# Kernel tuning notes

Measured on AMD Instinct MI355X. Metric: run time of the kernel, lower is better.

The kernel has to match this reference:

```python
import jax, jax.numpy as jnp
import numpy as np

B, S, I, H, C = 256, 128, 512, 1024, 10
VOCAB = S  # nn.Embedding(seq_length, input_dim)


def _lstm_dir(embeds_tbi, W, b):
    """Run an LSTM over time. embeds_tbi: [S,B,I]; W: [4H, I+H] stacked (g,i,f,o); b: [4H]."""
    h0 = jnp.zeros((B, H), jnp.float32)
    c0 = jnp.zeros((B, H), jnp.float32)

    def step(carry, x_t):
        c, h = carry
        xh = jnp.concatenate([x_t, h], axis=1)          # [B, I+H]
        z = xh @ W.T + b                                 # [B, 4H]
        g, i, f, o = jnp.split(z, 4, axis=1)
        g = jnp.tanh(g)
        i = jax.nn.sigmoid(i)
        f = jax.nn.sigmoid(f)
        o = jax.nn.sigmoid(o)
        new_c = g * i + c * f
        new_h = jnp.tanh(new_c) * o
        return (new_c, new_h), None

    (c_T, h_T), _ = jax.lax.scan(step, (c0, h0), embeds_tbi)
    return h_T


def setup_inputs() -> dict:
    key = jax.random.key(0)
    ks = jax.random.split(key, 8)
    x = jax.random.randint(ks[0], (B, S), 0, VOCAB)
    embed = jax.random.normal(ks[1], (VOCAB, I), jnp.float32) * 0.5
    scale = 1.0 / np.sqrt(I + H)
    fwd_W = jax.random.normal(ks[2], (4 * H, I + H), jnp.float32) * scale  # stacked g,i,f,o
    fwd_b = jax.random.normal(ks[3], (4 * H,), jnp.float32) * 0.02
    bwd_W = jax.random.normal(ks[4], (4 * H, I + H), jnp.float32) * scale
    bwd_b = jax.random.normal(ks[5], (4 * H,), jnp.float32) * 0.02
    p_w = jax.random.normal(ks[6], (C, 2 * H), jnp.float32) * (1.0 / np.sqrt(2 * H))
    p_b = jax.random.normal(ks[7], (C,), jnp.float32) * 0.02
    return {"x": x, "embed": embed, "fwd_W": fwd_W, "fwd_b": fwd_b,
            "bwd_W": bwd_W, "bwd_b": bwd_b, "p_w": p_w, "p_b": p_b}


def reference(x, embed, fwd_W, fwd_b, bwd_W, bwd_b, p_w, p_b):
    embeds = embed[x]                       # [B,S,I]
    emb_t = jnp.transpose(embeds, (1, 0, 2))  # [S,B,I]
    h_fwd = _lstm_dir(emb_t, fwd_W, fwd_b)
    h_bwd = _lstm_dir(emb_t[::-1], bwd_W, bwd_b)
    h_comb = jnp.concatenate([h_fwd, h_bwd], axis=1)  # [B,2H]
    return jax.nn.log_softmax(h_comb @ p_w.T + p_b, axis=1)
```

## Files before the change

### kernel.cpp

```cpp
#include <hip/hip_runtime.h>
#include <hip/hip_bf16.h>
#include <math.h>

#define B 256
#define S 128
#define I_DIM 512
#define H 1024
#define C 10
#define WROW 1536

#define LDS_H 131072

typedef float f32x4 __attribute__((ext_vector_type(4), may_alias));
typedef __bf16 bf16x8 __attribute__((ext_vector_type(8), may_alias));
typedef unsigned int u32x4 __attribute__((ext_vector_type(4), may_alias));
typedef unsigned long long u64;
typedef unsigned long long __attribute__((may_alias)) u64a;

__device__ __forceinline__ unsigned short f2bf(float f) {
    union { float f; unsigned u; } a; a.f = f;
    return (unsigned short)((a.u + 0x7fffu + ((a.u >> 16) & 1u)) >> 16);
}
__device__ __forceinline__ float bf2f(unsigned short b) {
    union { unsigned u; float f; } a; a.u = ((unsigned)b) << 16;
    return a.f;
}
__device__ __forceinline__ float sigf(float v) { return 1.0f / (1.0f + __expf(-v)); }
__device__ __forceinline__ float tanh_fast(float v) { return 1.0f - 2.0f / (1.0f + __expf(2.0f * v)); }

__global__ void wf_build(const float* __restrict__ fwd_W,
                         const float* __restrict__ bwd_W,
                         __hip_bfloat16* __restrict__ wF) {
    int gid = blockIdx.x * 256 + threadIdx.x;
    int lane = gid & 63, kk = (gid >> 6) & 31, nsub = (gid >> 11) & 255, d = gid >> 19;
    int n_gl = nsub * 16 + (lane & 15);
    int j = n_gl >> 2, g = n_gl & 3;
    int k = kk * 32 + (lane >> 4) * 8;
    const float* W = d ? bwd_W : fwd_W;
    const float* src = W + (size_t)(g * 1024 + j) * WROW + I_DIM + k;
    ushort4 lo = make_ushort4(f2bf(src[0]), f2bf(src[1]), f2bf(src[2]), f2bf(src[3]));
    ushort4 hi = make_ushort4(f2bf(src[4]), f2bf(src[5]), f2bf(src[6]), f2bf(src[7]));
    ushort4* dst = (ushort4*)(wF + (size_t)gid * 8);
    dst[0] = lo; dst[1] = hi;
}

__global__ void wxf_build(const float* __restrict__ fwd_W,
                          const float* __restrict__ bwd_W,
                          __hip_bfloat16* __restrict__ wxF) {
    int gid = blockIdx.x * 256 + threadIdx.x;
    int lane = gid & 63, kk = (gid >> 6) & 15, nsub = (gid >> 10) & 255, d = gid >> 18;
    int n_gl = nsub * 16 + (lane & 15);
    int j = n_gl >> 2, g = n_gl & 3;
    int k = kk * 32 + (lane >> 4) * 8;
    const float* W = d ? bwd_W : fwd_W;
    const float* src = W + (size_t)(g * 1024 + j) * WROW + k;
    ushort4 lo = make_ushort4(f2bf(src[0]), f2bf(src[1]), f2bf(src[2]), f2bf(src[3]));
    ushort4 hi = make_ushort4(f2bf(src[4]), f2bf(src[5]), f2bf(src[6]), f2bf(src[7]));
    ushort4* dst = (ushort4*)(wxF + (size_t)gid * 8);
    dst[0] = lo; dst[1] = hi;
}

__global__ void ehl_build(const float* __restrict__ embed,
                          unsigned short* __restrict__ ehl) {
    int idx = blockIdx.x * 256 + threadIdx.x;
    float e = embed[idx];
    unsigned short hb = f2bf(e);
    unsigned short lb = f2bf(e - bf2f(hb));
    ehl[idx] = hb;
    ehl[65536 + idx] = lb;
}

__global__ __launch_bounds__(256) void projp_mfma(
        const __hip_bfloat16* __restrict__ wxF,
        const unsigned short* __restrict__ ehl,
        const float* __restrict__ fwd_b,
        const float* __restrict__ bwd_b,
        float* __restrict__ projP) {
    extern __shared__ char sm[];
    const int bid = blockIdx.x;
    const int d = bid >> 7, jt = (bid >> 2) & 31, vb = bid & 3;
    const int tid = threadIdx.x, w = tid >> 6, lane = tid & 63;
    const int l15 = lane & 15, l4 = lane >> 4;
    const int v0 = vb * 32;

    for (int i = 0; i < 16; i++) {
        int chunk = i * 256 + tid;
        int row = chunk >> 6, c16 = chunk & 63;
        int p = row >> 5, vs = v0 + (row & 31);
        u32x4 vd = *(const u32x4*)(ehl + ((size_t)p * 128 + vs) * 512 + c16 * 8);
        *(u32x4*)(sm + row * 1024 + ((c16 * 16) ^ ((row & 7) << 4))) = vd;
    }
    __syncthreads();

    const __hip_bfloat16* ap0 = wxF + ((size_t)((d * 256 + jt * 8 + w * 2 + 0) * 16)) * 512;
    const __hip_bfloat16* ap1 = wxF + ((size_t)((d * 256 + jt * 8 + w * 2 + 1) * 16)) * 512;
    int hrow[2], hswz[2], lrow[2], lswz[2];
#pragma unroll
    for (int vt = 0; vt < 2; vt++) {
        int hr = vt * 16 + l15, lr = hr + 32;
        hrow[vt] = hr * 1024; hswz[vt] = (hr & 7) << 4;
        lrow[vt] = lr * 1024; lswz[vt] = (lr & 7) << 4;
    }
    f32x4 acc[2][2] = {};
#pragma unroll
    for (int kk = 0; kk < 16; kk++) {
        bf16x8 A0 = *(const bf16x8*)(ap0 + kk * 512 + lane * 8);
        bf16x8 A1 = *(const bf16x8*)(ap1 + kk * 512 + lane * 8);
        int ko = kk * 64 + l4 * 16;
        bf16x8 Bh0 = *(const bf16x8*)(sm + hrow[0] + (ko ^ hswz[0]));
        bf16x8 Bh1 = *(const bf16x8*)(sm + hrow[1] + (ko ^ hswz[1]));
        bf16x8 Bl0 = *(const bf16x8*)(sm + lrow[0] + (ko ^ lswz[0]));
        bf16x8 Bl1 = *(const bf16x8*)(sm + lrow[1] + (ko ^ lswz[1]));
        acc[0][0] = __builtin_amdgcn_mfma_f32_16x16x32_bf16(A0, Bh0, acc[0][0], 0, 0, 0);
        acc[0][0] = __builtin_amdgcn_mfma_f32_16x16x32_bf16(A0, Bl0, acc[0][0], 0, 0, 0);
        acc[0][1] = __builtin_amdgcn_mfma_f32_16x16x32_bf16(A0, Bh1, acc[0][1], 0, 0, 0);
        acc[0][1] = __builtin_amdgcn_mfma_f32_16x16x32_bf16(A0, Bl1, acc[0][1], 0, 0, 0);
        acc[1][0] = __builtin_amdgcn_mfma_f32_16x16x32_bf16(A1, Bh0, acc[1][0], 0, 0, 0);
        acc[1][0] = __builtin_amdgcn_mfma_f32_16x16x32_bf16(A1, Bl0, acc[1][0], 0, 0, 0);
        acc[1][1] = __builtin_amdgcn_mfma_f32_16x16x32_bf16(A1, Bh1, acc[1][1], 0, 0, 0);
        acc[1][1] = __builtin_amdgcn_mfma_f32_16x16x32_bf16(A1, Bl1, acc[1][1], 0, 0, 0);
    }
    const float* bp = d ? bwd_b : fwd_b;
#pragma unroll
    for (int nt = 0; nt < 2; nt++) {
        int j = jt * 32 + w * 8 + nt * 4 + l4;
        f32x4 bv = { bp[j], bp[1024 + j], bp[2048 + j], bp[3072 + j] };
#pragma unroll
        for (int vt = 0; vt < 2; vt++) {
            int v = v0 + vt * 16 + l15;
            *(f32x4*)(projP + ((size_t)(d * 1024 + j) * 128 + v) * 4) = acc[nt][vt] + bv;
        }
    }
}

__global__ __launch_bounds__(512, 1) void step_kernel(
        const int* __restrict__ x,
        const __hip_bfloat16* __restrict__ wF,
        const float* __restrict__ projP,
        __hip_bfloat16* __restrict__ hbuf,
        float* __restrict__ cws,
        int t) {
    extern __shared__ char smem[];
    const int bid = blockIdx.x;
    const int d = bid >> 7, bt = (bid >> 5) & 3, jt = bid & 31;
    const int tid = threadIdx.x, wid = tid >> 6, lane = tid & 63;
    const int l15 = lane & 15, l4 = lane >> 4;
    const int b0 = bt * 64;
    const size_t dBH = (size_t)d * B * H;

    if (t > 0) {
        const __hip_bfloat16* hr = hbuf + (size_t)(t & 1) * 2 * B * H + dBH + (size_t)b0 * H;
#pragma unroll
        for (int i = 0; i < 16; i++) {
            int flat = i * 512 + tid;
            int row = flat >> 7, c16 = flat & 127;
            u32x4 v = *(const u32x4*)(hr + (size_t)row * H + c16 * 8);
            *(u32x4*)(smem + row * 2048 + ((c16 * 16) ^ ((row & 7) << 4))) = v;
        }
        __syncthreads();
    }

    f32x4 acc[4] = {};
    if (t > 0) {
        const __hip_bfloat16* wp = wF + (size_t)(d * 256 + jt * 8 + wid) * 16384;
        int brow[4], bswz[4];
#pragma unroll
        for (int bs = 0; bs < 4; bs++) {
            int row = bs * 16 + l15;
            brow[bs] = row * 2048;
            bswz[bs] = (row & 7) << 4;
        }
        bf16x8 Acur = *(const bf16x8*)(wp + lane * 8);
        bf16x8 Bcur[4];
#pragma unroll
        for (int bs = 0; bs < 4; bs++)
            Bcur[bs] = *(const bf16x8*)(smem + brow[bs] + ((l4 * 16) ^ bswz[bs]));
#pragma unroll
        for (int kk = 0; kk < 32; kk++) {
            bf16x8 A = Acur;
            bf16x8 B0 = Bcur[0], B1 = Bcur[1], B2 = Bcur[2], B3 = Bcur[3];
            if (kk < 31) {
                Acur = *(const bf16x8*)(wp + (kk + 1) * 512 + lane * 8);
                int koff = (kk + 1) * 64 + l4 * 16;
#pragma unroll
                for (int bs = 0; bs < 4; bs++)
                    Bcur[bs] = *(const bf16x8*)(smem + brow[bs] + (koff ^ bswz[bs]));
            }
            acc[0] = __builtin_amdgcn_mfma_f32_16x16x32_bf16(A, B0, acc[0], 0, 0, 0);
            acc[1] = __builtin_amdgcn_mfma_f32_16x16x32_bf16(A, B1, acc[1], 0, 0, 0);
            acc[2] = __builtin_amdgcn_mfma_f32_16x16x32_bf16(A, B2, acc[2], 0, 0, 0);
            acc[3] = __builtin_amdgcn_mfma_f32_16x16x32_bf16(A, B3, acc[3], 0, 0, 0);
        }
    }

    const int tt = d ? (S - 1 - t) : t;
    const int j = jt * 32 + wid * 4 + l4;
    const f32x4* pp = (const f32x4*)projP + ((size_t)d * 1024 + j) * 128;
    f32x4 pj[4];
#pragma unroll
    for (int bs = 0; bs < 4; bs++) {
        int v = x[(b0 + bs * 16 + l15) * S + tt];
        pj[bs] = pp[v];
    }

    float* cp = cws + ((size_t)bid * 512 + tid) * 4;
    f32x4 cv = {0.f, 0.f, 0.f, 0.f};
    if (t > 0) cv = *(const f32x4*)cp;

    float hnv[4];
#pragma unroll
    for (int bs = 0; bs < 4; bs++) {
        float zg = acc[bs][0] + pj[bs][0];
        float zi = acc[bs][1] + pj[bs][1];
        float zf = acc[bs][2] + pj[bs][2];
        float zo = acc[bs][3] + pj[bs][3];
        float gg = tanh_fast(zg);
        float ii = sigf(zi);
        float ff = sigf(zf);
        float oo = sigf(zo);
        float cn = gg * ii + cv[bs] * ff;
        cv[bs] = cn;
        hnv[bs] = tanh_fast(cn) * oo;
    }
    *(f32x4*)cp = cv;

    unsigned plo = (unsigned)f2bf(hnv[0]) | ((unsigned)f2bf(hnv[1]) << 16);
    unsigned phi = (unsigned)f2bf(hnv[2]) | ((unsigned)f2bf(hnv[3]) << 16);
    unsigned short o4[4];
#pragma unroll
    for (int p = 0; p < 4; p++) {
        int src = p * 16 + l15;
        unsigned vlo = __shfl(plo, src);
        unsigned vhi = __shfl(phi, src);
        unsigned sel = (l4 < 2) ? vlo : vhi;
        o4[p] = (l4 & 1) ? (unsigned short)(sel >> 16) : (unsigned short)(sel & 0xffffu);
    }
    u64 hv = (u64)o4[0] | ((u64)o4[1] << 16) | ((u64)o4[2] << 32) | ((u64)o4[3] << 48);
    __hip_bfloat16* hw = hbuf + (size_t)((t + 1) & 1) * 2 * B * H + dBH
                         + (size_t)(b0 + lane) * H + jt * 32 + wid * 4;
    *(u64a*)hw = hv;
}

__global__ void head_kernel(const __hip_bfloat16* __restrict__ hbuf,
                            const float* __restrict__ p_w,
                            const float* __restrict__ p_b,
                            float* __restrict__ out) {
    int b = blockIdx.x;
    int lane = threadIdx.x;
    float part[C];
#pragma unroll
    for (int cc = 0; cc < C; cc++) part[cc] = 0.0f;
    for (int jj = lane; jj < 2 * H; jj += 64) {
        float hv = (jj < H)
            ? __bfloat162float(hbuf[(size_t)b * H + jj])
            : __bfloat162float(hbuf[(size_t)B * H + (size_t)b * H + jj - H]);
#pragma unroll
        for (int cc = 0; cc < C; cc++) part[cc] += hv * p_w[cc * 2 * H + jj];
    }
#pragma unroll
    for (int cc = 0; cc < C; cc++) {
        float v = part[cc];
        for (int off = 32; off; off >>= 1) v += __shfl_down(v, off);
        part[cc] = v;
    }
    if (lane == 0) {
        float lg[C];
        float m = -1e30f;
        for (int cc = 0; cc < C; cc++) {
            lg[cc] = part[cc] + p_b[cc];
            m = fmaxf(m, lg[cc]);
        }
        float s = 0.0f;
        for (int cc = 0; cc < C; cc++) s += expf(lg[cc] - m);
        float lse = logf(s) + m;
        for (int cc = 0; cc < C; cc++) out[b * C + cc] = lg[cc] - lse;
    }
}

extern "C" void kernel_launch(void* const* d_in, const int* in_sizes, int n_in,
                              void* d_out, int out_size, void* d_ws, size_t ws_size,
                              hipStream_t stream) {
    const int*   x     = (const int*)d_in[0];
    const float* embed = (const float*)d_in[1];
    const float* fwd_W = (const float*)d_in[2];
    const float* fwd_b = (const float*)d_in[3];
    const float* bwd_W = (const float*)d_in[4];
    const float* bwd_b = (const float*)d_in[5];
    const float* p_w   = (const float*)d_in[6];
    const float* p_b   = (const float*)d_in[7];
    float* outp = (float*)d_out;

    char* ws = (char*)d_ws;
    __hip_bfloat16* wF  = (__hip_bfloat16*)ws;  ws += (size_t)2 * 256 * 16384 * 2;
    __hip_bfloat16* wxF = (__hip_bfloat16*)ws;
    float* cws = (float*)ws;                    ws += (size_t)2 * 256 * 8192 * 2;
    unsigned short* ehl = (unsigned short*)ws;  ws += (size_t)2 * 128 * 512 * 2;
    float* projP = (float*)ws;                  ws += (size_t)2 * 1024 * 128 * 4 * 4;
    __hip_bfloat16* hbuf = (__hip_bfloat16*)ws; ws += (size_t)2 * 2 * B * H * 2;

    hipLaunchKernelGGL(wf_build, dim3(4096), dim3(256), 0, stream, fwd_W, bwd_W, wF);
    hipLaunchKernelGGL(wxf_build, dim3(2048), dim3(256), 0, stream, fwd_W, bwd_W, wxF);
    hipLaunchKernelGGL(ehl_build, dim3(256), dim3(256), 0, stream, embed, ehl);

    hipFuncSetAttribute((const void*)projp_mfma,
                        hipFuncAttributeMaxDynamicSharedMemorySize, 65536);
    hipLaunchKernelGGL(projp_mfma, dim3(256), dim3(256), 65536, stream,
                       wxF, ehl, fwd_b, bwd_b, projP);

    hipFuncSetAttribute((const void*)step_kernel,
                        hipFuncAttributeMaxDynamicSharedMemorySize, LDS_H);
    for (int t = 0; t < S; t++)
        hipLaunchKernelGGL(step_kernel, dim3(256), dim3(512), LDS_H, stream,
                           x, wF, projP, hbuf, cws, t);

    hipLaunchKernelGGL(head_kernel, dim3(B), dim3(64), 0, stream,
                       hbuf, p_w, p_b, outp);
}
```

Measured before the change: 1.431 ms.

## Load hidden state directly to LDS and merge prep kernels into one launch

The step kernel now stages the previous hidden-state tile into LDS with global_load_lds, which loads straight from global memory into LDS and skips the trip through registers. The XOR swizzle moves from the LDS write address to the global read address, because the direct-to-LDS path writes contiguous lane slots. The three weight/embedding preparation kernels are merged into one launch to save launch overhead. The step-kernel change runs 128 times and is the main target, but it relies on the builtin's LDS addressing semantics matching the assumed layout.

```diff
diff --git a/kernel.cpp b/kernel.cpp
--- a/kernel.cpp
+++ b/kernel.cpp
@@ -28,46 +28,44 @@
 __device__ __forceinline__ float sigf(float v) { return 1.0f / (1.0f + __expf(-v)); }
 __device__ __forceinline__ float tanh_fast(float v) { return 1.0f - 2.0f / (1.0f + __expf(2.0f * v)); }
 
-__global__ void wf_build(const float* __restrict__ fwd_W,
-                         const float* __restrict__ bwd_W,
-                         __hip_bfloat16* __restrict__ wF) {
+__global__ void prep_build(const float* __restrict__ fwd_W,
+                           const float* __restrict__ bwd_W,
+                           const float* __restrict__ embed,
+                           __hip_bfloat16* __restrict__ wF,
+                           __hip_bfloat16* __restrict__ wxF,
+                           unsigned short* __restrict__ ehl) {
     int gid = blockIdx.x * 256 + threadIdx.x;
-    int lane = gid & 63, kk = (gid >> 6) & 31, nsub = (gid >> 11) & 255, d = gid >> 19;
-    int n_gl = nsub * 16 + (lane & 15);
-    int j = n_gl >> 2, g = n_gl & 3;
-    int k = kk * 32 + (lane >> 4) * 8;
-    const float* W = d ? bwd_W : fwd_W;
-    const float* src = W + (size_t)(g * 1024 + j) * WROW + I_DIM + k;
-    ushort4 lo = make_ushort4(f2bf(src[0]), f2bf(src[1]), f2bf(src[2]), f2bf(src[3]));
-    ushort4 hi = make_ushort4(f2bf(src[4]), f2bf(src[5]), f2bf(src[6]), f2bf(src[7]));
-    ushort4* dst = (ushort4*)(wF + (size_t)gid * 8);
-    dst[0] = lo; dst[1] = hi;
-}
-
-__global__ void wxf_build(const float* __restrict__ fwd_W,
-                          const float* __restrict__ bwd_W,
-                          __hip_bfloat16* __restrict__ wxF) {
-    int gid = blockIdx.x * 256 + threadIdx.x;
-    int lane = gid & 63, kk = (gid >> 6) & 15, nsub = (gid >> 10) & 255, d = gid >> 18;
-    int n_gl = nsub * 16 + (lane & 15);
-    int j = n_gl >> 2, g = n_gl & 3;
-    int k = kk * 32 + (lane >> 4) * 8;
-    const float* W = d ? bwd_W : fwd_W;
-    const float* src = W + (size_t)(g * 1024 + j) * WROW + k;
-    ushort4 lo = make_ushort4(f2bf(src[0]), f2bf(src[1]), f2bf(src[2]), f2bf(src[3]));
-    ushort4 hi = make_ushort4(f2bf(src[4]), f2bf(src[5]), f2bf(src[6]), f2bf(src[7]));
-    ushort4* dst = (ushort4*)(wxF + (size_t)gid * 8);
-    dst[0] = lo; dst[1] = hi;
-}
-
-__global__ void ehl_build(const float* __restrict__ embed,
-                          unsigned short* __restrict__ ehl) {
-    int idx = blockIdx.x * 256 + threadIdx.x;
-    float e = embed[idx];
-    unsigned short hb = f2bf(e);
-    unsigned short lb = f2bf(e - bf2f(hb));
-    ehl[idx] = hb;
-    ehl[65536 + idx] = lb;
+    if (gid < 1048576) {
+        int lane = gid & 63, kk = (gid >> 6) & 31, nsub = (gid >> 11) & 255, d = gid >> 19;
+        int n_gl = nsub * 16 + (lane & 15);
+        int j = n_gl >> 2, g = n_gl & 3;
+        int k = kk * 32 + (lane >> 4) * 8;
+        const float* W = d ? bwd_W : fwd_W;
+        const float* src = W + (size_t)(g * 1024 + j) * WROW + I_DIM + k;
+        ushort4 lo = make_ushort4(f2bf(src[0]), f2bf(src[1]), f2bf(src[2]), f2bf(src[3]));
+        ushort4 hi = make_ushort4(f2bf(src[4]), f2bf(src[5]), f2bf(src[6]), f2bf(src[7]));
+        ushort4* dst = (ushort4*)(wF + (size_t)gid * 8);
+        dst[0] = lo; dst[1] = hi;
+    } else if (gid < 1048576 + 524288) {
+        int g2 = gid - 1048576;
+        int lane = g2 & 63, kk = (g2 >> 6) & 15, nsub = (g2 >> 10) & 255, d = g2 >> 18;
+        int n_gl = nsub * 16 + (lane & 15);
+        int j = n_gl >> 2, g = n_gl & 3;
+        int k = kk * 32 + (lane >> 4) * 8;
+        const float* W = d ? bwd_W : fwd_W;
+        const float* src = W + (size_t)(g * 1024 + j) * WROW + k;
+        ushort4 lo = make_ushort4(f2bf(src[0]), f2bf(src[1]), f2bf(src[2]), f2bf(src[3]));
+        ushort4 hi = make_ushort4(f2bf(src[4]), f2bf(src[5]), f2bf(src[6]), f2bf(src[7]));
+        ushort4* dst = (ushort4*)(wxF + (size_t)g2 * 8);
+        dst[0] = lo; dst[1] = hi;
+    } else {
+        int idx = gid - (1048576 + 524288);
+        float e = embed[idx];
+        unsigned short hb = f2bf(e);
+        unsigned short lb = f2bf(e - bf2f(hb));
+        ehl[idx] = hb;
+        ehl[65536 + idx] = lb;
+    }
 }
 
 __global__ __launch_bounds__(256) void projp_mfma(
@@ -149,14 +147,28 @@
     const size_t dBH = (size_t)d * B * H;
 
     if (t > 0) {
-        const __hip_bfloat16* hr = hbuf + (size_t)(t & 1) * 2 * B * H + dBH + (size_t)b0 * H;
+        const char* hrb = (const char*)(hbuf + (size_t)(t & 1) * 2 * B * H + dBH + (size_t)b0 * H);
+#if __has_builtin(__builtin_amdgcn_global_load_lds)
+#pragma unroll
+        for (int i = 0; i < 16; i++) {
+            int r = i * 8 + wid;
+            int row = r >> 1, half = r & 1;
+            int m = half * 64 + lane;
+            const void* src = hrb + row * 2048 + ((m ^ (row & 7)) << 4);
+            __builtin_amdgcn_global_load_lds(
+                (const __attribute__((address_space(1))) void*)src,
+                (__attribute__((address_space(3))) void*)(smem + row * 2048 + half * 1024),
+                16, 0, 0);
+        }
+#else
 #pragma unroll
         for (int i = 0; i < 16; i++) {
             int flat = i * 512 + tid;
             int row = flat >> 7, c16 = flat & 127;
-            u32x4 v = *(const u32x4*)(hr + (size_t)row * H + c16 * 8);
+            u32x4 v = *(const u32x4*)(hrb + (size_t)row * 2048 + c16 * 16);
             *(u32x4*)(smem + row * 2048 + ((c16 * 16) ^ ((row & 7) << 4))) = v;
         }
+#endif
         __syncthreads();
     }
 
@@ -298,9 +310,8 @@
     float* projP = (float*)ws;                  ws += (size_t)2 * 1024 * 128 * 4 * 4;
     __hip_bfloat16* hbuf = (__hip_bfloat16*)ws; ws += (size_t)2 * 2 * B * H * 2;
 
-    hipLaunchKernelGGL(wf_build, dim3(4096), dim3(256), 0, stream, fwd_W, bwd_W, wF);
-    hipLaunchKernelGGL(wxf_build, dim3(2048), dim3(256), 0, stream, fwd_W, bwd_W, wxF);
-    hipLaunchKernelGGL(ehl_build, dim3(256), dim3(256), 0, stream, embed, ehl);
+    hipLaunchKernelGGL(prep_build, dim3(6400), dim3(256), 0, stream,
+                       fwd_W, bwd_W, embed, wF, wxF, ehl);
 
     hipFuncSetAttribute((const void*)projp_mfma,
                         hipFuncAttributeMaxDynamicSharedMemorySize, 65536);
```

Result: no change. 1.414 ms, median of 2 (-1.2%).
